# Kernel tuning notes

Measured on AMD Instinct MI355X. Metric: run time of the kernel, lower is better.

## Reference

```python
import jax, jax.numpy as jnp
import numpy as np

# Standard JPEG luminance quantization table, transposed as in the original DiffJPEG repo.
_Y_TABLE = np.array([
    [16, 11, 10, 16, 24, 40, 51, 61],
    [12, 12, 14, 19, 26, 58, 60, 55],
    [14, 13, 16, 24, 40, 57, 69, 56],
    [14, 17, 22, 29, 51, 87, 80, 62],
    [18, 22, 37, 56, 68, 109, 103, 77],
    [24, 35, 55, 64, 81, 104, 113, 92],
    [49, 64, 78, 87, 103, 121, 120, 101],
    [72, 92, 95, 98, 112, 100, 103, 99]], dtype=np.float32).T

_n = np.arange(8)
_C = np.cos((2 * _n[:, None] + 1) * _n[None, :] * np.pi / 16)  # [spatial, freq]
_DCT_T = (_C[:, None, :, None] * _C[None, :, None, :]).astype(np.float32)
# IDCT basis: tensor[x,y,u,v] = cos((2u+1)x pi/16) cos((2v+1)y pi/16) (contract over x,y = freq)
_IDCT_T = (_C.T[:, None, :, None] * _C.T[None, :, None, :]).astype(np.float32)
_alpha = np.array([1.0 / np.sqrt(2)] + [1.0] * 7, dtype=np.float32)
_SCALE = (np.outer(_alpha, _alpha) * 0.25).astype(np.float32)   # DCT scale
_ALPHA = np.outer(_alpha, _alpha).astype(np.float32)            # IDCT alpha

_QUALITY = 80.0
_FACTOR = (200.0 - _QUALITY * 2) / 100.0  # = 0.4 (quality >= 50 branch)


def _diff_round(x):
    r = jnp.round(x)
    return r + (x - r) ** 3


def setup_inputs() -> dict:
    key = jax.random.key(0)
    x = jax.random.uniform(key, (8, 3, 1024, 1024), dtype=jnp.float32)
    return {"x": x}


def reference(x):
    k = 8
    B, C, H, W = x.shape
    y_tab = jnp.asarray(_Y_TABLE) * _FACTOR
    dct_t = jnp.asarray(_DCT_T)
    idct_t = jnp.asarray(_IDCT_T)
    scale = jnp.asarray(_SCALE)
    alpha = jnp.asarray(_ALPHA)

    img = x * 255.0
    # Block split: [B,C,H,W] -> [B,C,nblocks,8,8] (row-major block order, as torch code)
    blocks = img.reshape(B, C, H // k, k, W // k, k)
    blocks = blocks.transpose(0, 1, 2, 4, 3, 5).reshape(B, C, -1, k, k)

    # DCT (note: this repo applies y_table quantization to all 3 channels)
    dct = scale * jnp.einsum('bcnxy,xyuv->bcnuv', blocks - 128.0, dct_t)
    q = _diff_round(dct / y_tab)
    y, cb, cr = q[:, 0], q[:, 1], q[:, 2]

    # Dequantize + IDCT
    deq = q * y_tab
    sp = 0.25 * jnp.einsum('bcnuv,uvxy->bcnxy', deq * alpha, idct_t) + 128.0

    # Block merge back to [B,C,H,W]
    rec = sp.reshape(B, C, H // k, W // k, k, k)
    rec = rec.transpose(0, 1, 2, 4, 3, 5).reshape(B, C, H, W)
    rec = jnp.clip(rec, 0.0, 255.0) / 255.0
    return (y, cb, cr, rec)
```

## Files before the change

### kernel.cpp

```cpp
#include <hip/hip_runtime.h>
#include <cstddef>

#define CD1 0.9807852804032304
#define CD2 0.9238795325112867
#define CD3 0.8314696123025452
#define CD4 0.7071067811865476
#define CD5 0.5555702330196022
#define CD6 0.3826834323650898
#define CD7 0.19509032201612825

__device__ const int YLg[64] = {
  16,11,10,16,24,40,51,61,
  12,12,14,19,26,58,60,55,
  14,13,16,24,40,57,69,56,
  14,17,22,29,51,87,80,62,
  18,22,37,56,68,109,103,77,
  24,35,55,64,81,104,113,92,
  49,64,78,87,103,121,120,101,
  72,92,95,98,112,100,103,99
};

__global__ __launch_bounds__(256) void diffjpeg_kernel(const float* __restrict__ in,
                                                       float* __restrict__ out)
{
    __shared__ float lds[2304];

    const float CT[8][8] = {
      {1.0f,(float)CD1,(float)CD2,(float)CD3,(float)CD4,(float)CD5,(float)CD6,(float)CD7},
      {1.0f,(float)CD3,(float)CD6,(float)(-CD7),(float)(-CD4),(float)(-CD1),(float)(-CD2),(float)(-CD5)},
      {1.0f,(float)CD5,(float)(-CD6),(float)(-CD1),(float)(-CD4),(float)CD7,(float)CD2,(float)CD3},
      {1.0f,(float)CD7,(float)(-CD2),(float)(-CD5),(float)CD4,(float)CD3,(float)(-CD6),(float)(-CD1)},
      {1.0f,(float)(-CD7),(float)(-CD2),(float)CD5,(float)CD4,(float)(-CD3),(float)(-CD6),(float)CD1},
      {1.0f,(float)(-CD5),(float)(-CD6),(float)CD1,(float)(-CD4),(float)(-CD7),(float)CD2,(float)(-CD3)},
      {1.0f,(float)(-CD3),(float)CD6,(float)CD7,(float)(-CD4),(float)CD1,(float)(-CD2),(float)CD5},
      {1.0f,(float)(-CD1),(float)CD2,(float)(-CD3),(float)CD4,(float)(-CD5),(float)CD6,(float)(-CD7)}
    };

    const int tid = threadIdx.x;
    const int wg  = blockIdx.x;
    const int bc  = wg >> 9;
    const int rem = wg & 511;
    const int bh  = rem >> 2;
    const int bwq = (rem & 3) * 32;
    const int ch  = bc % 3;
    const int bb  = bc / 3;

    const size_t ibase = (size_t)bc * 1048576 + (size_t)bh * 8192 + (size_t)bwq * 8;

    if (tid < 64) {
        const int u = tid >> 3, v = tid & 7;
        const double a_u = u ? 1.0 : 0.7071067811865476;
        const double a_v = v ? 1.0 : 0.7071067811865476;
        const double qt  = (double)YLg[v * 8 + u] * 0.4;
        const double al  = a_u * a_v;
        lds[2176 + tid] = (float)(al * 0.25 / qt);
        lds[2240 + tid] = (float)(qt * al * 0.25);
    }

#pragma unroll
    for (int j = 0; j < 2; ++j) {
        const int flat = j * 1024 + tid * 4;
        const int r = flat >> 8, c = flat & 255;
        const float4 val = *reinterpret_cast<const float4*>(in + ibase + (size_t)r * 1024 + c);
        *reinterpret_cast<float4*>(&lds[r * 260 + c]) = val;
    }
    __syncthreads();

    const int blk = tid >> 3;
    const int p   = tid & 7;

    float d1[8];
    {
        const float4 m0 = *reinterpret_cast<const float4*>(&lds[p * 260 + blk * 8]);
        const float4 m1 = *reinterpret_cast<const float4*>(&lds[p * 260 + blk * 8 + 4]);
        float s[8] = {m0.x, m0.y, m0.z, m0.w, m1.x, m1.y, m1.z, m1.w};
#pragma unroll
        for (int y = 0; y < 8; ++y) s[y] = fmaf(s[y], 255.0f, -128.0f);
#pragma unroll
        for (int v = 0; v < 8; ++v) {
            float acc = 0.0f;
#pragma unroll
            for (int y = 0; y < 8; ++y) acc = fmaf(s[y], CT[y][v], acc);
            d1[v] = acc;
        }
    }
    __syncthreads();
    *reinterpret_cast<float4*>(&lds[blk * 68 + p * 8])     = make_float4(d1[0], d1[1], d1[2], d1[3]);
    *reinterpret_cast<float4*>(&lds[blk * 68 + p * 8 + 4]) = make_float4(d1[4], d1[5], d1[6], d1[7]);
    __syncthreads();

    float q[8], dq[8];
    {
        float c0[8];
#pragma unroll
        for (int x = 0; x < 8; ++x) c0[x] = lds[blk * 68 + x * 8 + p];
#pragma unroll
        for (int u = 0; u < 8; ++u) {
            float acc = 0.0f;
#pragma unroll
            for (int x = 0; x < 8; ++x) acc = fmaf(CT[x][u], c0[x], acc);
            const float kq = lds[2176 + u * 8 + p];
            const float kd = lds[2240 + u * 8 + p];
            const float xq = acc * kq;
            const float r  = rintf(xq);
            const float d  = xq - r;
            q[u]  = r + d * d * d;
            dq[u] = q[u] * kd;
        }
#pragma unroll
        for (int u = 0; u < 8; ++u) lds[blk * 68 + u * 8 + p] = q[u];
    }
    __syncthreads();

    {
        float* qb = out + (size_t)ch * 8388608 + (size_t)bb * 1048576
                        + ((size_t)(bh * 128) + bwq) * 64;
#pragma unroll
        for (int j = 0; j < 2; ++j) {
            const int flat = j * 1024 + tid * 4;
            const int rec = flat >> 6, off = flat & 63;
            const float4 val = *reinterpret_cast<const float4*>(&lds[rec * 68 + off]);
            *reinterpret_cast<float4*>(qb + flat) = val;
        }
    }

    float e1[8];
#pragma unroll
    for (int x = 0; x < 8; ++x) {
        float acc = 0.0f;
#pragma unroll
        for (int u = 0; u < 8; ++u) acc = fmaf(CT[x][u], dq[u], acc);
        e1[x] = acc;
    }
    __syncthreads();
#pragma unroll
    for (int x = 0; x < 8; ++x) lds[blk * 68 + x * 8 + p] = e1[x];
    __syncthreads();

    float orow[8];
    {
        const float4 a0 = *reinterpret_cast<const float4*>(&lds[blk * 68 + p * 8]);
        const float4 a1 = *reinterpret_cast<const float4*>(&lds[blk * 68 + p * 8 + 4]);
        const float e[8] = {a0.x, a0.y, a0.z, a0.w, a1.x, a1.y, a1.z, a1.w};
#pragma unroll
        for (int y = 0; y < 8; ++y) {
            float acc = 0.0f;
#pragma unroll
            for (int v = 0; v < 8; ++v) acc = fmaf(e[v], CT[y][v], acc);
            acc += 128.0f;
            acc = fminf(fmaxf(acc, 0.0f), 255.0f);
            orow[y] = acc * (1.0f / 255.0f);
        }
    }
    __syncthreads();
    *reinterpret_cast<float4*>(&lds[p * 260 + blk * 8])     = make_float4(orow[0], orow[1], orow[2], orow[3]);
    *reinterpret_cast<float4*>(&lds[p * 260 + blk * 8 + 4]) = make_float4(orow[4], orow[5], orow[6], orow[7]);
    __syncthreads();

    {
        float* rb = out + (size_t)25165824 + (size_t)bc * 1048576
                        + (size_t)bh * 8192 + (size_t)bwq * 8;
#pragma unroll
        for (int j = 0; j < 2; ++j) {
            const int flat = j * 1024 + tid * 4;
            const int r = flat >> 8, c = flat & 255;
            const float4 val = *reinterpret_cast<const float4*>(&lds[r * 260 + c]);
            *reinterpret_cast<float4*>(rb + (size_t)r * 1024 + c) = val;
        }
    }
}

extern "C" void kernel_launch(void* const* d_in, const int* in_sizes, int n_in,
                              void* d_out, int out_size, void* d_ws, size_t ws_size,
                              hipStream_t stream) {
    const float* x = (const float*)d_in[0];
    float*       o = (float*)d_out;
    diffjpeg_kernel<<<12288, 256, 0, stream>>>(x, o);
}
```

Baseline: 53.07 us.

## Read input and write reconstruction directly from registers, cutting LDS staging and barriers

Each thread now loads its 8-pixel row straight from global memory and writes the reconstructed row straight back, instead of staging whole tiles through LDS. Quantized coefficients go to a separate LDS region so the column IDCT can run in the same phase as quantization. This drops several __syncthreads and LDS round trips. The cost is less coalesced global access: each thread touches two float4s 32 bytes apart, and lanes stride across rows 4 KB apart. LDS usage grows to about 17.5 KB per block.

```diff
diff --git a/kernel.cpp b/kernel.cpp
--- a/kernel.cpp
+++ b/kernel.cpp
@@ -23,7 +23,7 @@
 __global__ __launch_bounds__(256) void diffjpeg_kernel(const float* __restrict__ in,
                                                        float* __restrict__ out)
 {
-    __shared__ float lds[2304];
+    __shared__ float lds[4480];
 
     const float CT[8][8] = {
       {1.0f,(float)CD1,(float)CD2,(float)CD3,(float)CD4,(float)CD5,(float)CD6,(float)CD7},
@@ -45,34 +45,16 @@
     const int ch  = bc % 3;
     const int bb  = bc / 3;
 
-    const size_t ibase = (size_t)bc * 1048576 + (size_t)bh * 8192 + (size_t)bwq * 8;
-
-    if (tid < 64) {
-        const int u = tid >> 3, v = tid & 7;
-        const double a_u = u ? 1.0 : 0.7071067811865476;
-        const double a_v = v ? 1.0 : 0.7071067811865476;
-        const double qt  = (double)YLg[v * 8 + u] * 0.4;
-        const double al  = a_u * a_v;
-        lds[2176 + tid] = (float)(al * 0.25 / qt);
-        lds[2240 + tid] = (float)(qt * al * 0.25);
-    }
-
-#pragma unroll
-    for (int j = 0; j < 2; ++j) {
-        const int flat = j * 1024 + tid * 4;
-        const int r = flat >> 8, c = flat & 255;
-        const float4 val = *reinterpret_cast<const float4*>(in + ibase + (size_t)r * 1024 + c);
-        *reinterpret_cast<float4*>(&lds[r * 260 + c]) = val;
-    }
-    __syncthreads();
-
     const int blk = tid >> 3;
     const int p   = tid & 7;
 
+    const size_t ibase = (size_t)bc * 1048576 + (size_t)bh * 8192 + (size_t)bwq * 8;
+
     float d1[8];
     {
-        const float4 m0 = *reinterpret_cast<const float4*>(&lds[p * 260 + blk * 8]);
-        const float4 m1 = *reinterpret_cast<const float4*>(&lds[p * 260 + blk * 8 + 4]);
+        const float* src = in + ibase + (size_t)p * 1024 + blk * 8;
+        const float4 m0 = *reinterpret_cast<const float4*>(src);
+        const float4 m1 = *reinterpret_cast<const float4*>(src + 4);
         float s[8] = {m0.x, m0.y, m0.z, m0.w, m1.x, m1.y, m1.z, m1.w};
 #pragma unroll
         for (int y = 0; y < 8; ++y) s[y] = fmaf(s[y], 255.0f, -128.0f);
@@ -84,31 +66,47 @@
             d1[v] = acc;
         }
     }
-    __syncthreads();
+
+    if (tid < 64) {
+        const int u = tid >> 3, v = tid & 7;
+        const double a_u = u ? 1.0 : 0.7071067811865476;
+        const double a_v = v ? 1.0 : 0.7071067811865476;
+        const double qt  = (double)YLg[v * 8 + u] * 0.4;
+        const double al  = a_u * a_v;
+        lds[4352 + tid] = (float)(al * 0.25 / qt);
+        lds[4416 + tid] = (float)(qt * al * 0.25);
+    }
+
     *reinterpret_cast<float4*>(&lds[blk * 68 + p * 8])     = make_float4(d1[0], d1[1], d1[2], d1[3]);
     *reinterpret_cast<float4*>(&lds[blk * 68 + p * 8 + 4]) = make_float4(d1[4], d1[5], d1[6], d1[7]);
     __syncthreads();
 
-    float q[8], dq[8];
     {
         float c0[8];
 #pragma unroll
         for (int x = 0; x < 8; ++x) c0[x] = lds[blk * 68 + x * 8 + p];
+        float dq[8];
 #pragma unroll
         for (int u = 0; u < 8; ++u) {
             float acc = 0.0f;
 #pragma unroll
             for (int x = 0; x < 8; ++x) acc = fmaf(CT[x][u], c0[x], acc);
-            const float kq = lds[2176 + u * 8 + p];
-            const float kd = lds[2240 + u * 8 + p];
+            const float kq = lds[4352 + u * 8 + p];
+            const float kd = lds[4416 + u * 8 + p];
             const float xq = acc * kq;
             const float r  = rintf(xq);
             const float d  = xq - r;
-            q[u]  = r + d * d * d;
-            dq[u] = q[u] * kd;
+            const float qv = r + d * d * d;
+            lds[2176 + blk * 68 + u * 8 + p] = qv;
+            dq[u] = qv * kd;
         }
 #pragma unroll
-        for (int u = 0; u < 8; ++u) lds[blk * 68 + u * 8 + p] = q[u];
+        for (int x = 0; x < 8; ++x) {
+            float acc = 0.0f;
+#pragma unroll
+            for (int u = 0; u < 8; ++u) acc = fmaf(CT[x][u], dq[u], acc);
+            lds[blk * 68 + x * 8 + p] = acc;
+        }
     }
     __syncthreads();
 
@@ -119,29 +117,16 @@
         for (int j = 0; j < 2; ++j) {
             const int flat = j * 1024 + tid * 4;
             const int rec = flat >> 6, off = flat & 63;
-            const float4 val = *reinterpret_cast<const float4*>(&lds[rec * 68 + off]);
+            const float4 val = *reinterpret_cast<const float4*>(&lds[2176 + rec * 68 + off]);
             *reinterpret_cast<float4*>(qb + flat) = val;
         }
     }
 
-    float e1[8];
-#pragma unroll
-    for (int x = 0; x < 8; ++x) {
-        float acc = 0.0f;
-#pragma unroll
-        for (int u = 0; u < 8; ++u) acc = fmaf(CT[x][u], dq[u], acc);
-        e1[x] = acc;
-    }
-    __syncthreads();
-#pragma unroll
-    for (int x = 0; x < 8; ++x) lds[blk * 68 + x * 8 + p] = e1[x];
-    __syncthreads();
-
-    float orow[8];
     {
         const float4 a0 = *reinterpret_cast<const float4*>(&lds[blk * 68 + p * 8]);
         const float4 a1 = *reinterpret_cast<const float4*>(&lds[blk * 68 + p * 8 + 4]);
         const float e[8] = {a0.x, a0.y, a0.z, a0.w, a1.x, a1.y, a1.z, a1.w};
+        float orow[8];
 #pragma unroll
         for (int y = 0; y < 8; ++y) {
             float acc = 0.0f;
@@ -151,22 +136,9 @@
             acc = fminf(fmaxf(acc, 0.0f), 255.0f);
             orow[y] = acc * (1.0f / 255.0f);
         }
-    }
-    __syncthreads();
-    *reinterpret_cast<float4*>(&lds[p * 260 + blk * 8])     = make_float4(orow[0], orow[1], orow[2], orow[3]);
-    *reinterpret_cast<float4*>(&lds[p * 260 + blk * 8 + 4]) = make_float4(orow[4], orow[5], orow[6], orow[7]);
-    __syncthreads();
-
-    {
-        float* rb = out + (size_t)25165824 + (size_t)bc * 1048576
-                        + (size_t)bh * 8192 + (size_t)bwq * 8;
-#pragma unroll
-        for (int j = 0; j < 2; ++j) {
-            const int flat = j * 1024 + tid * 4;
-            const int r = flat >> 8, c = flat & 255;
-            const float4 val = *reinterpret_cast<const float4*>(&lds[r * 260 + c]);
-            *reinterpret_cast<float4*>(rb + (size_t)r * 1024 + c) = val;
-        }
+        float* rb = out + (size_t)25165824 + ibase + (size_t)p * 1024 + blk * 8;
+        *reinterpret_cast<float4*>(rb)     = make_float4(orow[0], orow[1], orow[2], orow[3]);
+        *reinterpret_cast<float4*>(rb + 4) = make_float4(orow[4], orow[5], orow[6], orow[7]);
     }
 }
 
```

After: 58.10 us. 9.5% more time.

## Use separate LDS regions to cut barriers and load input directly to LDS

Applied to the files above, without the earlier changes.

Gives the input, the intermediate coefficients and the quantized output their own LDS regions, so most of the write-after-read barriers between stages can be dropped and the inverse column transform is folded into the quantize step. The input tile is loaded with global_load_lds (direct global-to-LDS DMA) and no longer passes through registers. LDS use grows from about 9KB to about 26KB per workgroup, which may lower occupancy. The direct-to-LDS path also relies on the 16-byte variant being supported and on its address layout matching the padded destination.

```diff
diff --git a/kernel.cpp b/kernel.cpp
--- a/kernel.cpp
+++ b/kernel.cpp
@@ -23,7 +23,7 @@
 __global__ __launch_bounds__(256) void diffjpeg_kernel(const float* __restrict__ in,
                                                        float* __restrict__ out)
 {
-    __shared__ float lds[2304];
+    __shared__ float lds[6560];
 
     const float CT[8][8] = {
       {1.0f,(float)CD1,(float)CD2,(float)CD3,(float)CD4,(float)CD5,(float)CD6,(float)CD7},
@@ -45,7 +45,20 @@
     const int ch  = bc % 3;
     const int bb  = bc / 3;
 
+    const int blk = tid >> 3;
+    const int p   = tid & 7;
+
     const size_t ibase = (size_t)bc * 1048576 + (size_t)bh * 8192 + (size_t)bwq * 8;
+
+#pragma unroll
+    for (int j = 0; j < 2; ++j) {
+        const int flat = j * 1024 + tid * 4;
+        const int r = flat >> 8, c = flat & 255;
+        __builtin_amdgcn_global_load_lds(
+            (const __attribute__((address_space(1))) void*)(in + ibase + (size_t)r * 1024 + c),
+            (__attribute__((address_space(3))) void*)(&lds[r * 260 + c]),
+            16, 0, 0);
+    }
 
     if (tid < 64) {
         const int u = tid >> 3, v = tid & 7;
@@ -53,27 +66,16 @@
         const double a_v = v ? 1.0 : 0.7071067811865476;
         const double qt  = (double)YLg[v * 8 + u] * 0.4;
         const double al  = a_u * a_v;
-        lds[2176 + tid] = (float)(al * 0.25 / qt);
-        lds[2240 + tid] = (float)(qt * al * 0.25);
-    }
-
-#pragma unroll
-    for (int j = 0; j < 2; ++j) {
-        const int flat = j * 1024 + tid * 4;
-        const int r = flat >> 8, c = flat & 255;
-        const float4 val = *reinterpret_cast<const float4*>(in + ibase + (size_t)r * 1024 + c);
-        *reinterpret_cast<float4*>(&lds[r * 260 + c]) = val;
+        lds[6432 + tid] = (float)(al * 0.25 / qt);
+        lds[6496 + tid] = (float)(qt * al * 0.25);
     }
     __syncthreads();
 
-    const int blk = tid >> 3;
-    const int p   = tid & 7;
-
-    float d1[8];
     {
         const float4 m0 = *reinterpret_cast<const float4*>(&lds[p * 260 + blk * 8]);
         const float4 m1 = *reinterpret_cast<const float4*>(&lds[p * 260 + blk * 8 + 4]);
         float s[8] = {m0.x, m0.y, m0.z, m0.w, m1.x, m1.y, m1.z, m1.w};
+        float d1[8];
 #pragma unroll
         for (int y = 0; y < 8; ++y) s[y] = fmaf(s[y], 255.0f, -128.0f);
 #pragma unroll
@@ -83,32 +85,37 @@
             for (int y = 0; y < 8; ++y) acc = fmaf(s[y], CT[y][v], acc);
             d1[v] = acc;
         }
+        *reinterpret_cast<float4*>(&lds[2080 + blk * 68 + p * 8])     = make_float4(d1[0], d1[1], d1[2], d1[3]);
+        *reinterpret_cast<float4*>(&lds[2080 + blk * 68 + p * 8 + 4]) = make_float4(d1[4], d1[5], d1[6], d1[7]);
     }
     __syncthreads();
-    *reinterpret_cast<float4*>(&lds[blk * 68 + p * 8])     = make_float4(d1[0], d1[1], d1[2], d1[3]);
-    *reinterpret_cast<float4*>(&lds[blk * 68 + p * 8 + 4]) = make_float4(d1[4], d1[5], d1[6], d1[7]);
-    __syncthreads();
 
-    float q[8], dq[8];
     {
         float c0[8];
 #pragma unroll
-        for (int x = 0; x < 8; ++x) c0[x] = lds[blk * 68 + x * 8 + p];
+        for (int x = 0; x < 8; ++x) c0[x] = lds[2080 + blk * 68 + x * 8 + p];
+        float dq[8];
 #pragma unroll
         for (int u = 0; u < 8; ++u) {
             float acc = 0.0f;
 #pragma unroll
             for (int x = 0; x < 8; ++x) acc = fmaf(CT[x][u], c0[x], acc);
-            const float kq = lds[2176 + u * 8 + p];
-            const float kd = lds[2240 + u * 8 + p];
+            const float kq = lds[6432 + u * 8 + p];
+            const float kd = lds[6496 + u * 8 + p];
             const float xq = acc * kq;
             const float r  = rintf(xq);
             const float d  = xq - r;
-            q[u]  = r + d * d * d;
-            dq[u] = q[u] * kd;
+            const float qv = r + d * d * d;
+            lds[4256 + blk * 68 + u * 8 + p] = qv;
+            dq[u] = qv * kd;
         }
 #pragma unroll
-        for (int u = 0; u < 8; ++u) lds[blk * 68 + u * 8 + p] = q[u];
+        for (int x = 0; x < 8; ++x) {
+            float acc = 0.0f;
+#pragma unroll
+            for (int u = 0; u < 8; ++u) acc = fmaf(CT[x][u], dq[u], acc);
+            lds[2080 + blk * 68 + x * 8 + p] = acc;
+        }
     }
     __syncthreads();
 
@@ -119,29 +126,16 @@
         for (int j = 0; j < 2; ++j) {
             const int flat = j * 1024 + tid * 4;
             const int rec = flat >> 6, off = flat & 63;
-            const float4 val = *reinterpret_cast<const float4*>(&lds[rec * 68 + off]);
+            const float4 val = *reinterpret_cast<const float4*>(&lds[4256 + rec * 68 + off]);
             *reinterpret_cast<float4*>(qb + flat) = val;
         }
     }
 
-    float e1[8];
-#pragma unroll
-    for (int x = 0; x < 8; ++x) {
-        float acc = 0.0f;
-#pragma unroll
-        for (int u = 0; u < 8; ++u) acc = fmaf(CT[x][u], dq[u], acc);
-        e1[x] = acc;
-    }
-    __syncthreads();
-#pragma unroll
-    for (int x = 0; x < 8; ++x) lds[blk * 68 + x * 8 + p] = e1[x];
-    __syncthreads();
-
-    float orow[8];
     {
-        const float4 a0 = *reinterpret_cast<const float4*>(&lds[blk * 68 + p * 8]);
-        const float4 a1 = *reinterpret_cast<const float4*>(&lds[blk * 68 + p * 8 + 4]);
+        const float4 a0 = *reinterpret_cast<const float4*>(&lds[2080 + blk * 68 + p * 8]);
+        const float4 a1 = *reinterpret_cast<const float4*>(&lds[2080 + blk * 68 + p * 8 + 4]);
         const float e[8] = {a0.x, a0.y, a0.z, a0.w, a1.x, a1.y, a1.z, a1.w};
+        float orow[8];
 #pragma unroll
         for (int y = 0; y < 8; ++y) {
             float acc = 0.0f;
@@ -151,15 +145,13 @@
             acc = fminf(fmaxf(acc, 0.0f), 255.0f);
             orow[y] = acc * (1.0f / 255.0f);
         }
+        *reinterpret_cast<float4*>(&lds[p * 260 + blk * 8])     = make_float4(orow[0], orow[1], orow[2], orow[3]);
+        *reinterpret_cast<float4*>(&lds[p * 260 + blk * 8 + 4]) = make_float4(orow[4], orow[5], orow[6], orow[7]);
     }
-    __syncthreads();
-    *reinterpret_cast<float4*>(&lds[p * 260 + blk * 8])     = make_float4(orow[0], orow[1], orow[2], orow[3]);
-    *reinterpret_cast<float4*>(&lds[p * 260 + blk * 8 + 4]) = make_float4(orow[4], orow[5], orow[6], orow[7]);
     __syncthreads();
 
     {
-        float* rb = out + (size_t)25165824 + (size_t)bc * 1048576
-                        + (size_t)bh * 8192 + (size_t)bwq * 8;
+        float* rb = out + (size_t)25165824 + ibase;
 #pragma unroll
         for (int j = 0; j < 2; ++j) {
             const int flat = j * 1024 + tid * 4;
```

Measured after the change: 53.14 us. About the same (+0.1%).
